# Kernel optimization log

Measured on AMD Instinct MI355X. Metric: run time of the kernel, lower is better.

## Reference

```python
import jax, jax.numpy as jnp
import numpy as np

N_NODES = 100000

def spmm(rows, cols, vals, x):
    # out[r] = sum_e vals[e] * x[cols[e]] for edges with rows[e] == r
    msgs = vals[:, None] * x[cols]            # [E, F]
    return jax.ops.segment_sum(msgs, rows, num_segments=N_NODES)

def setup_inputs() -> dict:
    key = jax.random.key(0)
    ks = jax.random.split(key, 8)
    N, E, F_IN, H, C = N_NODES, 1600000, 128, 128, 64
    x = jax.random.normal(ks[0], (N, F_IN), dtype=jnp.float32)
    edge_rows = jax.random.randint(ks[1], (E,), 0, N, dtype=jnp.int32)
    edge_cols = jax.random.randint(ks[2], (E,), 0, N, dtype=jnp.int32)
    edge_vals = jax.random.uniform(ks[3], (E,), dtype=jnp.float32)
    W1 = jax.random.normal(ks[4], (F_IN, H), dtype=jnp.float32) * (1.0 / np.sqrt(F_IN))
    b1 = jnp.zeros((H,), dtype=jnp.float32)
    W2 = jax.random.normal(ks[5], (H, C), dtype=jnp.float32) * (1.0 / np.sqrt(H))
    b2 = jnp.zeros((C,), dtype=jnp.float32)
    return {"x": x, "edge_rows": edge_rows, "edge_cols": edge_cols,
            "edge_vals": edge_vals, "W1": W1, "b1": b1, "W2": W2, "b2": b2}

def reference(x, edge_rows, edge_cols, edge_vals, W1, b1, W2, b2):
    # Layer 1: spmm(adj, x) then linear, then ReLU (dropout = identity at eval)
    h = spmm(edge_rows, edge_cols, edge_vals, x)   # [N, F_IN]
    h = h @ W1 + b1                                # [N, H]
    h = jax.nn.relu(h)
    # Layer 2
    h = spmm(edge_rows, edge_cols, edge_vals, h)   # [N, H]
    return h @ W2 + b2                             # [N, C]
```

## Files before the change

kernel.cpp:

```cpp
#include <hip/hip_runtime.h>


typedef __attribute__((ext_vector_type(8))) short short8;
typedef __attribute__((ext_vector_type(4))) float floatx4;

#define ELLS 64

static __device__ __forceinline__ unsigned short f2bf(float f) {
    unsigned int u = __builtin_bit_cast(unsigned int, f);
    u += 0x7fffu + ((u >> 16) & 1u);
    return (unsigned short)(u >> 16);
}
static __device__ __forceinline__ float bflo(unsigned int u) {
    return __builtin_bit_cast(float, u << 16);
}
static __device__ __forceinline__ float bfhi(unsigned int u) {
    return __builtin_bit_cast(float, u & 0xffff0000u);
}

__global__ __launch_bounds__(256) void prep_kernel(
    const float* __restrict__ W1, const float* __restrict__ W2,
    unsigned short* __restrict__ W1t, unsigned short* __restrict__ W2t,
    int* __restrict__ cursor, int N)
{
    int idx = blockIdx.x * 256 + threadIdx.x;
    if (idx < N) cursor[idx] = 0;
    if (idx < 128 * 128) {
        int n = idx >> 7, k = idx & 127;
        W1t[idx] = f2bf(W1[(size_t)k * 128 + n]);
    }
    if (idx < 64 * 128) {
        int n = idx >> 7, k = idx & 127;
        W2t[idx] = f2bf(W2[(size_t)k * 64 + n]);
    }
}

template<int OUT, bool AF32>
static __device__ __forceinline__ void gemm_mfma_body(
    const void* __restrict__ Av, const unsigned short* __restrict__ Wt,
    unsigned short* __restrict__ Y, int N, int bid)
{
    constexpr int NT = OUT / 16;
    const int lane = threadIdx.x & 63;
    const int wave = threadIdx.x >> 6;
    const int quad = lane >> 4;
    const int l16  = lane & 15;
    const int row0 = bid * 64 + wave * 16;
    int arow = row0 + l16;
    if (arow > N - 1) arow = N - 1;

    short8 af[4];
    if (AF32) {
        const float* ap = (const float*)Av + (size_t)arow * 128 + quad * 8;
        #pragma unroll
        for (int kt = 0; kt < 4; ++kt) {
            const float4* p = (const float4*)(ap + kt * 32);
            float4 lo = p[0], hi = p[1];
            short8 t;
            t[0] = (short)f2bf(lo.x); t[1] = (short)f2bf(lo.y);
            t[2] = (short)f2bf(lo.z); t[3] = (short)f2bf(lo.w);
            t[4] = (short)f2bf(hi.x); t[5] = (short)f2bf(hi.y);
            t[6] = (short)f2bf(hi.z); t[7] = (short)f2bf(hi.w);
            af[kt] = t;
        }
    } else {
        const unsigned short* ap =
            (const unsigned short*)Av + (size_t)arow * 128 + quad * 8;
        #pragma unroll
        for (int kt = 0; kt < 4; ++kt)
            af[kt] = *(const short8*)(ap + kt * 32);
    }

    floatx4 acc[NT];
    #pragma unroll
    for (int nt = 0; nt < NT; ++nt) acc[nt] = (floatx4){0.f, 0.f, 0.f, 0.f};

    #pragma unroll
    for (int nt = 0; nt < NT; ++nt) {
        const unsigned short* wp = Wt + (size_t)(nt * 16 + l16) * 128 + quad * 8;
        #pragma unroll
        for (int kt = 0; kt < 4; ++kt) {
            short8 bfr = *(const short8*)(wp + kt * 32);
            acc[nt] = __builtin_amdgcn_mfma_f32_16x16x32_bf16(
                af[kt], bfr, acc[nt], 0, 0, 0);
        }
    }

    #pragma unroll
    for (int nt = 0; nt < NT; ++nt) {
        int col = nt * 16 + l16;
        #pragma unroll
        for (int r = 0; r < 4; ++r) {
            int row = row0 + quad * 4 + r;
            if (row < N)
                Y[(size_t)row * OUT + col] = f2bf(acc[nt][r]);
        }
    }
}

__global__ __launch_bounds__(256) void fill_ell_gemm1_fused(
    const int* __restrict__ erow, const int* __restrict__ ecol,
    const float* __restrict__ eval, int* __restrict__ cursor,
    int2* __restrict__ ell, int E, int FB, int RSTEP,
    const float* __restrict__ x, const unsigned short* __restrict__ W1t,
    unsigned short* __restrict__ y1b, int N)
{
    if ((int)blockIdx.x < FB) {
        const int g     = blockIdx.x & 7;
        const int chunk = blockIdx.x >> 3;
        const int lo = g * RSTEP;
        const int hi = min(lo + RSTEP, N);
        int base = chunk * 1024 + (int)threadIdx.x * 4;
        if (base >= E) return;

        if (base + 4 <= E) {
            int4   r4 = *(const int4*)(erow + base);
            int4   c4 = *(const int4*)(ecol + base);
            float4 v4 = *(const float4*)(eval + base);
            int   rr[4] = {r4.x, r4.y, r4.z, r4.w};
            int   cc[4] = {c4.x, c4.y, c4.z, c4.w};
            float vv[4] = {v4.x, v4.y, v4.z, v4.w};
            #pragma unroll
            for (int j = 0; j < 4; ++j) {
                int r = rr[j];
                if (r >= lo && r < hi) {
                    int p = atomicAdd(&cursor[r], 1);
                    if (p < ELLS)
                        ell[((size_t)r << 6) + p] =
                            make_int2(cc[j], __float_as_int(vv[j]));
                }
            }
        } else {
            for (int j = 0; j < 4; ++j) {
                int e = base + j;
                if (e < E) {
                    int r = erow[e];
                    if (r >= lo && r < hi) {
                        int p = atomicAdd(&cursor[r], 1);
                        if (p < ELLS)
                            ell[((size_t)r << 6) + p] =
                                make_int2(ecol[e], __float_as_int(eval[e]));
                    }
                }
            }
        }
    } else {
        gemm_mfma_body<128, true>(x, W1t, y1b, N, blockIdx.x - FB);
    }
}

template<bool RELU>
__global__ __launch_bounds__(256) void spmm_gather128(
    const int* __restrict__ deg, const int2* __restrict__ ell,
    const unsigned short* __restrict__ xb,
    const float* __restrict__ bias, unsigned short* __restrict__ outb, int N)
{
    int row = (blockIdx.x * 256 + threadIdx.x) >> 6;
    if (row >= N) return;
    int lane = threadIdx.x & 63;
    const unsigned int* xf = (const unsigned int*)xb;

    int d = min(deg[row], ELLS);
    const int2* ep = ell + ((size_t)row << 6);

    float x0 = 0.f, y0 = 0.f, x1 = 0.f, y1 = 0.f;
    float x2 = 0.f, y2 = 0.f, x3 = 0.f, y3 = 0.f;
    int i = 0;
    for (; i + 3 < d; i += 4) {
        int2 cv0 = ep[i],     cv1 = ep[i + 1];
        int2 cv2 = ep[i + 2], cv3 = ep[i + 3];
        unsigned int u0 = xf[(size_t)cv0.x * 64 + lane];
        unsigned int u1 = xf[(size_t)cv1.x * 64 + lane];
        unsigned int u2 = xf[(size_t)cv2.x * 64 + lane];
        unsigned int u3 = xf[(size_t)cv3.x * 64 + lane];
        float v0 = __int_as_float(cv0.y), v1 = __int_as_float(cv1.y);
        float v2 = __int_as_float(cv2.y), v3 = __int_as_float(cv3.y);
        x0 = fmaf(v0, bflo(u0), x0);  y0 = fmaf(v0, bfhi(u0), y0);
        x1 = fmaf(v1, bflo(u1), x1);  y1 = fmaf(v1, bfhi(u1), y1);
        x2 = fmaf(v2, bflo(u2), x2);  y2 = fmaf(v2, bfhi(u2), y2);
        x3 = fmaf(v3, bflo(u3), x3);  y3 = fmaf(v3, bfhi(u3), y3);
    }
    for (; i < d; ++i) {
        int2 cv = ep[i];
        float v0 = __int_as_float(cv.y);
        unsigned int u0 = xf[(size_t)cv.x * 64 + lane];
        x0 = fmaf(v0, bflo(u0), x0);  y0 = fmaf(v0, bfhi(u0), y0);
    }
    float2 b = ((const float2*)bias)[lane];
    float sx = x0 + x1 + x2 + x3 + b.x;
    float sy = y0 + y1 + y2 + y3 + b.y;
    if (RELU) { sx = fmaxf(sx, 0.f); sy = fmaxf(sy, 0.f); }
    ((unsigned int*)outb)[(size_t)row * 64 + lane] =
        (unsigned int)f2bf(sx) | ((unsigned int)f2bf(sy) << 16);
}

__global__ __launch_bounds__(256) void spmm_gather64_out(
    const int* __restrict__ deg, const int2* __restrict__ ell,
    const unsigned short* __restrict__ y2b,
    const float* __restrict__ bias, float* __restrict__ out, int N)
{
    int row = (blockIdx.x * 256 + threadIdx.x) >> 6;
    if (row >= N) return;
    int lane = threadIdx.x & 63;
    int half = lane >> 5, fl = lane & 31;
    const unsigned int* xf = (const unsigned int*)y2b;

    int d = min(deg[row], ELLS);
    const int2* ep = ell + ((size_t)row << 6);

    float x0 = 0.f, y0 = 0.f, x1 = 0.f, y1 = 0.f;
    int i = half;
    for (; i + 2 < d; i += 4) {
        int2 cv0 = ep[i], cv1 = ep[i + 2];
        unsigned int u0 = xf[(size_t)cv0.x * 32 + fl];
        unsigned int u1 = xf[(size_t)cv1.x * 32 + fl];
        float v0 = __int_as_float(cv0.y), v1 = __int_as_float(cv1.y);
        x0 = fmaf(v0, bflo(u0), x0);  y0 = fmaf(v0, bfhi(u0), y0);
        x1 = fmaf(v1, bflo(u1), x1);  y1 = fmaf(v1, bfhi(u1), y1);
    }
    if (i < d) {
        int2 cv = ep[i];
        float v0 = __int_as_float(cv.y);
        unsigned int u0 = xf[(size_t)cv.x * 32 + fl];
        x0 = fmaf(v0, bflo(u0), x0);  y0 = fmaf(v0, bfhi(u0), y0);
    }
    float sx = x0 + x1, sy = y0 + y1;
    sx += __shfl_xor(sx, 32);
    sy += __shfl_xor(sy, 32);
    if (half == 0) {
        float2 b = ((const float2*)bias)[fl];
        ((float2*)out)[(size_t)row * 32 + fl] =
            make_float2(sx + b.x, sy + b.y);
    }
}

__global__ __launch_bounds__(256) void gemm2_mfma(
    const unsigned short* __restrict__ A, const unsigned short* __restrict__ Wt,
    unsigned short* __restrict__ Y, int N)
{
    gemm_mfma_body<64, false>(A, Wt, Y, N, blockIdx.x);
}

extern "C" void kernel_launch(void* const* d_in, const int* in_sizes, int n_in,
                              void* d_out, int out_size, void* d_ws, size_t ws_size,
                              hipStream_t stream)
{
    const float* x    = (const float*)d_in[0];
    const int*   erow = (const int*)  d_in[1];
    const int*   ecol = (const int*)  d_in[2];
    const float* eval = (const float*)d_in[3];
    const float* W1   = (const float*)d_in[4];
    const float* b1   = (const float*)d_in[5];
    const float* W2   = (const float*)d_in[6];
    const float* b2   = (const float*)d_in[7];
    float*       out  = (float*)d_out;

    const int N = in_sizes[0] / 128;
    const int E = in_sizes[1];
    const int NP = N + 64;

    unsigned short* y1b = (unsigned short*)d_ws;
    unsigned short* h2b = y1b + (size_t)NP * 128;
    unsigned short* y2b = h2b + (size_t)NP * 128;
    unsigned short* W1t = y2b + (size_t)NP * 64;
    unsigned short* W2t = W1t + 128 * 128;
    int2*  ell    = (int2*)(W2t + 64 * 128);
    int*   cursor = (int*)(ell + (size_t)N * ELLS);

    const int spmm_blocks = (N + 3) / 4;
    const int mfma_blocks = (N + 63) / 64;
    const int prep_blocks = (N + 255) / 256;
    const int RSTEP       = (N + 7) / 8;
    const int chunks      = (E + 1023) / 1024;
    const int FB          = 8 * chunks;

    prep_kernel<<<prep_blocks, 256, 0, stream>>>(W1, W2, W1t, W2t, cursor, N);

    fill_ell_gemm1_fused<<<FB + mfma_blocks, 256, 0, stream>>>(
        erow, ecol, eval, cursor, ell, E, FB, RSTEP, x, W1t, y1b, N);

    spmm_gather128<true><<<spmm_blocks, 256, 0, stream>>>(
        cursor, ell, y1b, b1, h2b, N);

    gemm2_mfma<<<mfma_blocks, 256, 0, stream>>>(h2b, W2t, y2b, N);
    spmm_gather64_out<<<spmm_blocks, 256, 0, stream>>>(
        cursor, ell, y2b, b2, out, N);
}
```

Baseline: 364.9 us.

## Fuse layer-1 SpMM gather with GEMM2 via shared-memory tile

Merges the 128-wide SpMM gather (with bias and ReLU) and the second MFMA GEMM into one kernel. Each 1024-thread block has 16 waves, each gathering one row into a padded LDS tile. After a barrier, four waves run the 16x64 MFMA against W2t and write y2b directly. This removes the h2b round trip through global memory and one kernel launch, at the cost of a block-wide barrier and three quarters of the waves idling during the GEMM phase.

```diff
diff --git a/kernel.cpp b/kernel.cpp
--- a/kernel.cpp
+++ b/kernel.cpp
@@ -5,6 +5,7 @@
 typedef __attribute__((ext_vector_type(4))) float floatx4;
 
 #define ELLS 64
+#define H2LD 136
 
 static __device__ __forceinline__ unsigned short f2bf(float f) {
     unsigned int u = __builtin_bit_cast(unsigned int, f);
@@ -35,12 +36,10 @@
     }
 }
 
-template<int OUT, bool AF32>
-static __device__ __forceinline__ void gemm_mfma_body(
-    const void* __restrict__ Av, const unsigned short* __restrict__ Wt,
+static __device__ __forceinline__ void gemm1_body(
+    const float* __restrict__ A, const unsigned short* __restrict__ Wt,
     unsigned short* __restrict__ Y, int N, int bid)
 {
-    constexpr int NT = OUT / 16;
     const int lane = threadIdx.x & 63;
     const int wave = threadIdx.x >> 6;
     const int quad = lane >> 4;
@@ -50,33 +49,25 @@
     if (arow > N - 1) arow = N - 1;
 
     short8 af[4];
-    if (AF32) {
-        const float* ap = (const float*)Av + (size_t)arow * 128 + quad * 8;
-        #pragma unroll
-        for (int kt = 0; kt < 4; ++kt) {
-            const float4* p = (const float4*)(ap + kt * 32);
-            float4 lo = p[0], hi = p[1];
-            short8 t;
-            t[0] = (short)f2bf(lo.x); t[1] = (short)f2bf(lo.y);
-            t[2] = (short)f2bf(lo.z); t[3] = (short)f2bf(lo.w);
-            t[4] = (short)f2bf(hi.x); t[5] = (short)f2bf(hi.y);
-            t[6] = (short)f2bf(hi.z); t[7] = (short)f2bf(hi.w);
-            af[kt] = t;
-        }
-    } else {
-        const unsigned short* ap =
-            (const unsigned short*)Av + (size_t)arow * 128 + quad * 8;
-        #pragma unroll
-        for (int kt = 0; kt < 4; ++kt)
-            af[kt] = *(const short8*)(ap + kt * 32);
-    }
-
-    floatx4 acc[NT];
+    const float* ap = A + (size_t)arow * 128 + quad * 8;
     #pragma unroll
-    for (int nt = 0; nt < NT; ++nt) acc[nt] = (floatx4){0.f, 0.f, 0.f, 0.f};
-
+    for (int kt = 0; kt < 4; ++kt) {
+        const float4* p = (const float4*)(ap + kt * 32);
+        float4 lo = p[0], hi = p[1];
+        short8 t;
+        t[0] = (short)f2bf(lo.x); t[1] = (short)f2bf(lo.y);
+        t[2] = (short)f2bf(lo.z); t[3] = (short)f2bf(lo.w);
+        t[4] = (short)f2bf(hi.x); t[5] = (short)f2bf(hi.y);
+        t[6] = (short)f2bf(hi.z); t[7] = (short)f2bf(hi.w);
+        af[kt] = t;
+    }
+
+    floatx4 acc[8];
     #pragma unroll
-    for (int nt = 0; nt < NT; ++nt) {
+    for (int nt = 0; nt < 8; ++nt) acc[nt] = (floatx4){0.f, 0.f, 0.f, 0.f};
+
+    #pragma unroll
+    for (int nt = 0; nt < 8; ++nt) {
         const unsigned short* wp = Wt + (size_t)(nt * 16 + l16) * 128 + quad * 8;
         #pragma unroll
         for (int kt = 0; kt < 4; ++kt) {
@@ -87,13 +78,13 @@
     }
 
     #pragma unroll
-    for (int nt = 0; nt < NT; ++nt) {
+    for (int nt = 0; nt < 8; ++nt) {
         int col = nt * 16 + l16;
         #pragma unroll
         for (int r = 0; r < 4; ++r) {
             int row = row0 + quad * 4 + r;
             if (row < N)
-                Y[(size_t)row * OUT + col] = f2bf(acc[nt][r]);
+                Y[(size_t)row * 128 + col] = f2bf(acc[nt][r]);
         }
     }
 }
@@ -145,53 +136,85 @@
             }
         }
     } else {
-        gemm_mfma_body<128, true>(x, W1t, y1b, N, blockIdx.x - FB);
-    }
-}
-
-template<bool RELU>
-__global__ __launch_bounds__(256) void spmm_gather128(
+        gemm1_body(x, W1t, y1b, N, blockIdx.x - FB);
+    }
+}
+
+__global__ __launch_bounds__(1024, 8) void spmm128_gemm2_fused(
     const int* __restrict__ deg, const int2* __restrict__ ell,
-    const unsigned short* __restrict__ xb,
-    const float* __restrict__ bias, unsigned short* __restrict__ outb, int N)
-{
-    int row = (blockIdx.x * 256 + threadIdx.x) >> 6;
-    if (row >= N) return;
-    int lane = threadIdx.x & 63;
-    const unsigned int* xf = (const unsigned int*)xb;
-
-    int d = min(deg[row], ELLS);
-    const int2* ep = ell + ((size_t)row << 6);
-
-    float x0 = 0.f, y0 = 0.f, x1 = 0.f, y1 = 0.f;
-    float x2 = 0.f, y2 = 0.f, x3 = 0.f, y3 = 0.f;
-    int i = 0;
-    for (; i + 3 < d; i += 4) {
-        int2 cv0 = ep[i],     cv1 = ep[i + 1];
-        int2 cv2 = ep[i + 2], cv3 = ep[i + 3];
-        unsigned int u0 = xf[(size_t)cv0.x * 64 + lane];
-        unsigned int u1 = xf[(size_t)cv1.x * 64 + lane];
-        unsigned int u2 = xf[(size_t)cv2.x * 64 + lane];
-        unsigned int u3 = xf[(size_t)cv3.x * 64 + lane];
-        float v0 = __int_as_float(cv0.y), v1 = __int_as_float(cv1.y);
-        float v2 = __int_as_float(cv2.y), v3 = __int_as_float(cv3.y);
-        x0 = fmaf(v0, bflo(u0), x0);  y0 = fmaf(v0, bfhi(u0), y0);
-        x1 = fmaf(v1, bflo(u1), x1);  y1 = fmaf(v1, bfhi(u1), y1);
-        x2 = fmaf(v2, bflo(u2), x2);  y2 = fmaf(v2, bfhi(u2), y2);
-        x3 = fmaf(v3, bflo(u3), x3);  y3 = fmaf(v3, bfhi(u3), y3);
-    }
-    for (; i < d; ++i) {
-        int2 cv = ep[i];
-        float v0 = __int_as_float(cv.y);
-        unsigned int u0 = xf[(size_t)cv.x * 64 + lane];
-        x0 = fmaf(v0, bflo(u0), x0);  y0 = fmaf(v0, bfhi(u0), y0);
-    }
-    float2 b = ((const float2*)bias)[lane];
-    float sx = x0 + x1 + x2 + x3 + b.x;
-    float sy = y0 + y1 + y2 + y3 + b.y;
-    if (RELU) { sx = fmaxf(sx, 0.f); sy = fmaxf(sy, 0.f); }
-    ((unsigned int*)outb)[(size_t)row * 64 + lane] =
-        (unsigned int)f2bf(sx) | ((unsigned int)f2bf(sy) << 16);
+    const unsigned short* __restrict__ y1b, const float* __restrict__ b1,
+    const unsigned short* __restrict__ W2t,
+    unsigned short* __restrict__ y2b, int N)
+{
+    __shared__ unsigned short h2s[16 * H2LD];
+
+    const int wave = threadIdx.x >> 6;
+    const int lane = threadIdx.x & 63;
+    const int row  = blockIdx.x * 16 + wave;
+
+    unsigned int pack = 0;
+    if (row < N) {
+        const unsigned int* xf = (const unsigned int*)y1b;
+        int d = min(deg[row], ELLS);
+        const int2* ep = ell + ((size_t)row << 6);
+
+        float x0 = 0.f, y0 = 0.f, x1 = 0.f, y1 = 0.f;
+        float x2 = 0.f, y2 = 0.f, x3 = 0.f, y3 = 0.f;
+        int i = 0;
+        for (; i + 3 < d; i += 4) {
+            int2 cv0 = ep[i],     cv1 = ep[i + 1];
+            int2 cv2 = ep[i + 2], cv3 = ep[i + 3];
+            unsigned int u0 = xf[(size_t)cv0.x * 64 + lane];
+            unsigned int u1 = xf[(size_t)cv1.x * 64 + lane];
+            unsigned int u2 = xf[(size_t)cv2.x * 64 + lane];
+            unsigned int u3 = xf[(size_t)cv3.x * 64 + lane];
+            float v0 = __int_as_float(cv0.y), v1 = __int_as_float(cv1.y);
+            float v2 = __int_as_float(cv2.y), v3 = __int_as_float(cv3.y);
+            x0 = fmaf(v0, bflo(u0), x0);  y0 = fmaf(v0, bfhi(u0), y0);
+            x1 = fmaf(v1, bflo(u1), x1);  y1 = fmaf(v1, bfhi(u1), y1);
+            x2 = fmaf(v2, bflo(u2), x2);  y2 = fmaf(v2, bfhi(u2), y2);
+            x3 = fmaf(v3, bflo(u3), x3);  y3 = fmaf(v3, bfhi(u3), y3);
+        }
+        for (; i < d; ++i) {
+            int2 cv = ep[i];
+            float v0 = __int_as_float(cv.y);
+            unsigned int u0 = xf[(size_t)cv.x * 64 + lane];
+            x0 = fmaf(v0, bflo(u0), x0);  y0 = fmaf(v0, bfhi(u0), y0);
+        }
+        float2 b = ((const float2*)b1)[lane];
+        float sx = fmaxf(x0 + x1 + x2 + x3 + b.x, 0.f);
+        float sy = fmaxf(y0 + y1 + y2 + y3 + b.y, 0.f);
+        pack = (unsigned int)f2bf(sx) | ((unsigned int)f2bf(sy) << 16);
+    }
+    ((unsigned int*)(h2s + wave * H2LD))[lane] = pack;
+    __syncthreads();
+
+    if (wave < 4) {
+        const int quad = lane >> 4;
+        const int l16  = lane & 15;
+        const int nt   = wave;
+
+        short8 af[4];
+        #pragma unroll
+        for (int kt = 0; kt < 4; ++kt)
+            af[kt] = *(const short8*)(h2s + l16 * H2LD + quad * 8 + kt * 32);
+
+        floatx4 acc = (floatx4){0.f, 0.f, 0.f, 0.f};
+        const unsigned short* wp = W2t + (size_t)(nt * 16 + l16) * 128 + quad * 8;
+        #pragma unroll
+        for (int kt = 0; kt < 4; ++kt) {
+            short8 bfr = *(const short8*)(wp + kt * 32);
+            acc = __builtin_amdgcn_mfma_f32_16x16x32_bf16(af[kt], bfr, acc, 0, 0, 0);
+        }
+
+        int col = nt * 16 + l16;
+        #pragma unroll
+        for (int r = 0; r < 4; ++r) {
+            int grow = blockIdx.x * 16 + quad * 4 + r;
+            if (grow < N)
+                y2b[(size_t)grow * 64 + col] = f2bf(acc[r]);
+        }
+    }
 }
 
 __global__ __launch_bounds__(256) void spmm_gather64_out(
@@ -234,13 +257,6 @@
     }
 }
 
-__global__ __launch_bounds__(256) void gemm2_mfma(
-    const unsigned short* __restrict__ A, const unsigned short* __restrict__ Wt,
-    unsigned short* __restrict__ Y, int N)
-{
-    gemm_mfma_body<64, false>(A, Wt, Y, N, blockIdx.x);
-}
-
 extern "C" void kernel_launch(void* const* d_in, const int* in_sizes, int n_in,
                               void* d_out, int out_size, void* d_ws, size_t ws_size,
                               hipStream_t stream)
@@ -260,29 +276,28 @@
     const int NP = N + 64;
 
     unsigned short* y1b = (unsigned short*)d_ws;
-    unsigned short* h2b = y1b + (size_t)NP * 128;
-    unsigned short* y2b = h2b + (size_t)NP * 128;
+    unsigned short* y2b = y1b + (size_t)NP * 128;
     unsigned short* W1t = y2b + (size_t)NP * 64;
     unsigned short* W2t = W1t + 128 * 128;
     int2*  ell    = (int2*)(W2t + 64 * 128);
     int*   cursor = (int*)(ell + (size_t)N * ELLS);
 
-    const int spmm_blocks = (N + 3) / 4;
-    const int mfma_blocks = (N + 63) / 64;
-    const int prep_blocks = (N + 255) / 256;
-    const int RSTEP       = (N + 7) / 8;
-    const int chunks      = (E + 1023) / 1024;
-    const int FB          = 8 * chunks;
+    const int spmm_blocks  = (N + 3) / 4;
+    const int fused_blocks = (N + 15) / 16;
+    const int mfma_blocks  = (N + 63) / 64;
+    const int prep_blocks  = (N + 255) / 256;
+    const int RSTEP        = (N + 7) / 8;
+    const int chunks       = (E + 1023) / 1024;
+    const int FB           = 8 * chunks;
 
     prep_kernel<<<prep_blocks, 256, 0, stream>>>(W1, W2, W1t, W2t, cursor, N);
 
     fill_ell_gemm1_fused<<<FB + mfma_blocks, 256, 0, stream>>>(
         erow, ecol, eval, cursor, ell, E, FB, RSTEP, x, W1t, y1b, N);
 
-    spmm_gather128<true><<<spmm_blocks, 256, 0, stream>>>(
-        cursor, ell, y1b, b1, h2b, N);
-
-    gemm2_mfma<<<mfma_blocks, 256, 0, stream>>>(h2b, W2t, y2b, N);
+    spmm128_gemm2_fused<<<fused_blocks, 1024, 0, stream>>>(
+        cursor, ell, y1b, b1, W2t, y2b, N);
+
     spmm_gather64_out<<<spmm_blocks, 256, 0, stream>>>(
         cursor, ell, y2b, b2, out, N);
 }
```

Result: no change. 361.6 us (-0.9%).
